# Optimization experiments

Measured on AMD Instinct MI355X. Metric: run time of the kernel, lower is better.

The kernel has to match this reference:

```python
import jax, jax.numpy as jnp
import numpy as np

K = 5  # adaptive kernel size; kernel has K*K channels


def setup_inputs() -> dict:
    key = jax.random.key(0)
    k1, k2 = jax.random.split(key)
    B, C, H, W = 8, 64, 256, 256
    x = jax.random.normal(k1, (B, C, H + K - 1, W + K - 1), dtype=jnp.float32)
    kernel = jax.random.uniform(k2, (B, K * K, H, W), dtype=jnp.float32)
    return {"x": x, "kernel": kernel}


def reference(x, kernel):
    # x: [B, C, H+K-1, W+K-1], kernel: [B, K*K, H, W] -> out: [B, C, H, W]
    # Each output pixel (h, w) = sum_{i,j} x[:, :, h+i, w+j] * kernel[:, i*K+j, h, w]
    B, KK, H, W = kernel.shape
    out = jnp.zeros((B, x.shape[1], H, W), dtype=x.dtype)
    for idx in range(KK):
        i, j = idx // K, idx % K
        patch = x[:, :, i:i + H, j:j + W]              # [B, C, H, W]
        out = out + patch * kernel[:, idx][:, None]    # broadcast tap over C
    return out
```

## Files before the change

### kernel.cpp

```cpp
#include <hip/hip_runtime.h>


constexpr int K  = 5;
constexpr int B  = 8;
constexpr int C  = 64;
constexpr int H  = 256;
constexpr int W  = 256;
constexpr int HX = H + K - 1;
constexpr int WX = W + K - 1;

constexpr int CH  = 8;
constexpr int NCG = C / CH;
constexpr int HPB = 4;
constexpr int NHB = H / HPB;
constexpr int NWG = NHB * B * NCG;

typedef float f4 __attribute__((ext_vector_type(4)));

__global__ __launch_bounds__(256, 3)
void adaptive_conv_kernel(const float* __restrict__ x,
                          const float* __restrict__ kern,
                          float* __restrict__ out) {
    const int k    = blockIdx.x;
    const int orig = (k & 7) * (NWG / 8) + (k >> 3);
    const int cg   = orig & (NCG - 1);
    const int hblk = (orig >> 3) & (NHB - 1);
    const int b    = orig >> 9;

    const int tid = threadIdx.x;
    const int wg  = tid & 63;
    const int hr  = tid >> 6;
    const int w0  = wg * 4;
    const int h   = hblk * HPB + hr;
    const int c0  = cg * CH;

    f4 acc[CH];
    #pragma unroll
    for (int ch = 0; ch < CH; ++ch) acc[ch] = (f4)0.0f;

    const float* xb = x    + ((size_t)b * C + c0) * (HX * WX) + (size_t)h * WX + w0;
    const float* kb = kern + (size_t)b * (K * K * H * W)      + (size_t)h * W  + w0;

    #pragma unroll
    for (int i = 0; i < K; ++i) {
        f4 t[K];
        #pragma unroll
        for (int j = 0; j < K; ++j) {
            t[j] = *(const f4*)(kb + (size_t)(i * K + j) * (H * W));
        }

        #pragma unroll
        for (int ch = 0; ch < CH; ++ch) {
            const float* xr = xb + (size_t)ch * (HX * WX) + (size_t)i * WX;
            f4 xa  = *(const f4*)(xr);
            f4 xcv = *(const f4*)(xr + 4);
            float xs[8] = {xa.x, xa.y, xa.z, xa.w, xcv.x, xcv.y, xcv.z, xcv.w};

            #pragma unroll
            for (int j = 0; j < K; ++j) {
                acc[ch].x = fmaf(xs[j + 0], t[j].x, acc[ch].x);
                acc[ch].y = fmaf(xs[j + 1], t[j].y, acc[ch].y);
                acc[ch].z = fmaf(xs[j + 2], t[j].z, acc[ch].z);
                acc[ch].w = fmaf(xs[j + 3], t[j].w, acc[ch].w);
            }
        }
    }

    float* ob = out + ((size_t)b * C + c0) * (H * W) + (size_t)h * W + w0;
    #pragma unroll
    for (int ch = 0; ch < CH; ++ch) {
        __builtin_nontemporal_store(acc[ch], (f4*)(ob + (size_t)ch * (H * W)));
    }
}

extern "C" void kernel_launch(void* const* d_in, const int* in_sizes, int n_in,
                              void* d_out, int out_size, void* d_ws, size_t ws_size,
                              hipStream_t stream) {
    const float* x    = (const float*)d_in[0];
    const float* kern = (const float*)d_in[1];
    float*       out  = (float*)d_out;

    dim3 grid(NWG);
    dim3 block(256);
    adaptive_conv_kernel<<<grid, block, 0, stream>>>(x, kern, out);
}
```

Measured before the change: 79.64 us.

## Stage input x tile with halo rows into LDS before convolution

Each workgroup now cooperatively copies its 8 input rows (4 output rows plus halo) for all 8 channels into shared memory, synchronizes, and then reads x taps from LDS instead of global memory. The aim is to cut repeated global and L1 traffic for the overlapping rows that the four wavefronts share. In exchange it uses about 66KB of LDS per block, lowers launch bounds occupancy from 3 to 2, and adds a barrier with no overlap between the load phase and compute.

```diff
diff --git a/kernel.cpp b/kernel.cpp
--- a/kernel.cpp
+++ b/kernel.cpp
@@ -15,31 +15,58 @@
 constexpr int NHB = H / HPB;
 constexpr int NWG = NHB * B * NCG;
 
+constexpr int XROWS     = HPB + K - 1;
+constexpr int CH_FLOATS = XROWS * WX;
+constexpr int LDS_FLOATS = CH * CH_FLOATS;
+
 typedef float f4 __attribute__((ext_vector_type(4)));
 
-__global__ __launch_bounds__(256, 3)
+__global__ __launch_bounds__(256, 2)
 void adaptive_conv_kernel(const float* __restrict__ x,
                           const float* __restrict__ kern,
                           float* __restrict__ out) {
+    __shared__ float xs[LDS_FLOATS];
+
     const int k    = blockIdx.x;
     const int orig = (k & 7) * (NWG / 8) + (k >> 3);
     const int cg   = orig & (NCG - 1);
     const int hblk = (orig >> 3) & (NHB - 1);
     const int b    = orig >> 9;
 
-    const int tid = threadIdx.x;
-    const int wg  = tid & 63;
-    const int hr  = tid >> 6;
-    const int w0  = wg * 4;
-    const int h   = hblk * HPB + hr;
-    const int c0  = cg * CH;
+    const int tid  = threadIdx.x;
+    const int lane = tid & 63;
+    const int wv   = tid >> 6;
+    const int w0   = lane * 4;
+    const int h    = hblk * HPB + wv;
+    const int c0   = cg * CH;
+
+    const size_t xplane = (size_t)HX * WX;
+    {
+        const float* xg0 = x + ((size_t)b * C + c0) * xplane
+                             + (size_t)(hblk * HPB) * WX;
+        #pragma unroll
+        for (int cc = 0; cc < 2; ++cc) {
+            const int ch = wv * 2 + cc;
+            const float* src = xg0 + (size_t)ch * xplane;
+            float*       dst = &xs[ch * CH_FLOATS];
+            #pragma unroll
+            for (int t = 0; t < 8; ++t) {
+                f4 v = *(const f4*)(src + t * 256 + lane * 4);
+                *(f4*)(dst + t * 256 + lane * 4) = v;
+            }
+            if (lane < 8) {
+                f4 v = *(const f4*)(src + 2048 + lane * 4);
+                *(f4*)(dst + 2048 + lane * 4) = v;
+            }
+        }
+    }
+    __syncthreads();
 
     f4 acc[CH];
     #pragma unroll
     for (int ch = 0; ch < CH; ++ch) acc[ch] = (f4)0.0f;
 
-    const float* xb = x    + ((size_t)b * C + c0) * (HX * WX) + (size_t)h * WX + w0;
-    const float* kb = kern + (size_t)b * (K * K * H * W)      + (size_t)h * W  + w0;
+    const float* kb = kern + (size_t)b * (K * K * H * W) + (size_t)h * W + w0;
 
     #pragma unroll
     for (int i = 0; i < K; ++i) {
@@ -51,17 +78,17 @@
 
         #pragma unroll
         for (int ch = 0; ch < CH; ++ch) {
-            const float* xr = xb + (size_t)ch * (HX * WX) + (size_t)i * WX;
+            const float* xr = &xs[ch * CH_FLOATS + (wv + i) * WX + w0];
             f4 xa  = *(const f4*)(xr);
             f4 xcv = *(const f4*)(xr + 4);
-            float xs[8] = {xa.x, xa.y, xa.z, xa.w, xcv.x, xcv.y, xcv.z, xcv.w};
+            float xsg[8] = {xa.x, xa.y, xa.z, xa.w, xcv.x, xcv.y, xcv.z, xcv.w};
 
             #pragma unroll
             for (int j = 0; j < K; ++j) {
-                acc[ch].x = fmaf(xs[j + 0], t[j].x, acc[ch].x);
-                acc[ch].y = fmaf(xs[j + 1], t[j].y, acc[ch].y);
-                acc[ch].z = fmaf(xs[j + 2], t[j].z, acc[ch].z);
-                acc[ch].w = fmaf(xs[j + 3], t[j].w, acc[ch].w);
+                acc[ch].x = fmaf(xsg[j + 0], t[j].x, acc[ch].x);
+                acc[ch].y = fmaf(xsg[j + 1], t[j].y, acc[ch].y);
+                acc[ch].z = fmaf(xsg[j + 2], t[j].z, acc[ch].z);
+                acc[ch].w = fmaf(xsg[j + 3], t[j].w, acc[ch].w);
             }
         }
     }
```

Result: faster. 66.49 us (-16.5%).

## Stage input halo tile in LDS and retile blocks to 8 rows by 128 columns

Applied to the files above, without the earlier changes.

Each block now cooperatively loads an 8-channel, 12-row, 132-column halo tile of x into shared memory and reads the 5x5 window from LDS instead of from global memory. Blocks are retiled to 8 output rows by 128 columns, which needs a new block-index decomposition. The goal is to remove the redundant global reads of overlapping x rows across the vertical taps. The costs are about 50KB of LDS per block, which may limit occupancy against the declared launch bounds of 3, and a synchronisation barrier with no overlap between staging and compute.

```diff
diff --git a/kernel.cpp b/kernel.cpp
--- a/kernel.cpp
+++ b/kernel.cpp
@@ -11,9 +11,15 @@
 
 constexpr int CH  = 8;
 constexpr int NCG = C / CH;
-constexpr int HPB = 4;
+constexpr int HPB = 8;
 constexpr int NHB = H / HPB;
-constexpr int NWG = NHB * B * NCG;
+constexpr int WPB = 128;
+constexpr int NWS = W / WPB;
+constexpr int NWG = NCG * NWS * NHB * B;
+
+constexpr int XR       = HPB + K - 1;
+constexpr int SROW_F4  = 34;
+constexpr int STAGE_F4 = CH * XR * 33;
 
 typedef float f4 __attribute__((ext_vector_type(4)));
 
@@ -21,25 +27,49 @@
 void adaptive_conv_kernel(const float* __restrict__ x,
                           const float* __restrict__ kern,
                           float* __restrict__ out) {
+    __shared__ float xs[CH][XR][SROW_F4 * 4];
+
     const int k    = blockIdx.x;
     const int orig = (k & 7) * (NWG / 8) + (k >> 3);
     const int cg   = orig & (NCG - 1);
-    const int hblk = (orig >> 3) & (NHB - 1);
+    const int ws   = (orig >> 3) & (NWS - 1);
+    const int hblk = (orig >> 4) & (NHB - 1);
     const int b    = orig >> 9;
 
     const int tid = threadIdx.x;
-    const int wg  = tid & 63;
-    const int hr  = tid >> 6;
-    const int w0  = wg * 4;
-    const int h   = hblk * HPB + hr;
+    const int r8  = tid >> 5;
+    const int cp  = tid & 31;
+    const int w0l = cp * 4;
+    const int wg0 = ws * WPB;
+    const int h   = hblk * HPB + r8;
     const int c0  = cg * CH;
+
+    const size_t xplane = (size_t)HX * WX;
+
+    {
+        const float* xg = x + ((size_t)b * C + c0) * xplane
+                            + (size_t)(hblk * HPB) * WX + wg0;
+        #pragma unroll
+        for (int it = 0; it < 13; ++it) {
+            const int idx = it * 256 + tid;
+            if (idx < STAGE_F4) {
+                const int ch  = idx / (XR * 33);
+                const int rem = idx - ch * (XR * 33);
+                const int rr  = rem / 33;
+                const int s   = rem - rr * 33;
+                f4 v = *(const f4*)(xg + (size_t)ch * xplane + rr * WX + s * 4);
+                *(f4*)&xs[ch][rr][s * 4] = v;
+            }
+        }
+    }
+    __syncthreads();
+
+    const float* kb = kern + (size_t)b * (K * K * H * W)
+                           + (size_t)h * W + wg0 + w0l;
 
     f4 acc[CH];
     #pragma unroll
     for (int ch = 0; ch < CH; ++ch) acc[ch] = (f4)0.0f;
-
-    const float* xb = x    + ((size_t)b * C + c0) * (HX * WX) + (size_t)h * WX + w0;
-    const float* kb = kern + (size_t)b * (K * K * H * W)      + (size_t)h * W  + w0;
 
     #pragma unroll
     for (int i = 0; i < K; ++i) {
@@ -51,22 +81,22 @@
 
         #pragma unroll
         for (int ch = 0; ch < CH; ++ch) {
-            const float* xr = xb + (size_t)ch * (HX * WX) + (size_t)i * WX;
-            f4 xa  = *(const f4*)(xr);
-            f4 xcv = *(const f4*)(xr + 4);
-            float xs[8] = {xa.x, xa.y, xa.z, xa.w, xcv.x, xcv.y, xcv.z, xcv.w};
+            const float* xr_ = &xs[ch][r8 + i][w0l];
+            f4 xa  = *(const f4*)(xr_);
+            f4 xcv = *(const f4*)(xr_ + 4);
+            float xsg[8] = {xa.x, xa.y, xa.z, xa.w, xcv.x, xcv.y, xcv.z, xcv.w};
 
             #pragma unroll
             for (int j = 0; j < K; ++j) {
-                acc[ch].x = fmaf(xs[j + 0], t[j].x, acc[ch].x);
-                acc[ch].y = fmaf(xs[j + 1], t[j].y, acc[ch].y);
-                acc[ch].z = fmaf(xs[j + 2], t[j].z, acc[ch].z);
-                acc[ch].w = fmaf(xs[j + 3], t[j].w, acc[ch].w);
+                acc[ch].x = fmaf(xsg[j + 0], t[j].x, acc[ch].x);
+                acc[ch].y = fmaf(xsg[j + 1], t[j].y, acc[ch].y);
+                acc[ch].z = fmaf(xsg[j + 2], t[j].z, acc[ch].z);
+                acc[ch].w = fmaf(xsg[j + 3], t[j].w, acc[ch].w);
             }
         }
     }
 
-    float* ob = out + ((size_t)b * C + c0) * (H * W) + (size_t)h * W + w0;
+    float* ob = out + ((size_t)b * C + c0) * (H * W) + (size_t)h * W + wg0 + w0l;
     #pragma unroll
     for (int ch = 0; ch < CH; ++ch) {
         __builtin_nontemporal_store(acc[ch], (f4*)(ob + (size_t)ch * (H * W)));
```

Result: faster. 66.03 us (-17.1%).
